# Kernel optimization log

Measured on AMD Instinct MI355X. Metric: run time of the kernel, lower is better.

The kernel has to match this reference:

```python
import jax, jax.numpy as jnp
import numpy as np

HIDDEN = 768
NUM_HEADS = 12
HEAD_DIM = HIDDEN // NUM_HEADS
B, S = 4, 2048


def setup_inputs() -> dict:
    key = jax.random.key(0)
    ks = jax.random.split(key, 10)
    scale = 1.0 / np.sqrt(HIDDEN)
    return {
        "hidden_states": jax.random.normal(ks[0], (B, S, HIDDEN), dtype=jnp.float32),
        "attention_mask": jnp.ones((B, S), dtype=jnp.float32),
        "Wq": jax.random.normal(ks[1], (HIDDEN, HIDDEN), dtype=jnp.float32) * scale,
        "bq": jnp.zeros((HIDDEN,), dtype=jnp.float32),
        "Wk": jax.random.normal(ks[2], (HIDDEN, HIDDEN), dtype=jnp.float32) * scale,
        "bk": jnp.zeros((HIDDEN,), dtype=jnp.float32),
        "Wv": jax.random.normal(ks[3], (HIDDEN, HIDDEN), dtype=jnp.float32) * scale,
        "bv": jnp.zeros((HIDDEN,), dtype=jnp.float32),
        "Wo": jax.random.normal(ks[4], (HIDDEN, HIDDEN), dtype=jnp.float32) * scale,
        "bo": jnp.zeros((HIDDEN,), dtype=jnp.float32),
    }


def reference(hidden_states, attention_mask, Wq, bq, Wk, bk, Wv, bv, Wo, bo):
    b, s, _ = hidden_states.shape
    # nn.Linear: x @ W.T + b  (W is [out, in])
    Q = hidden_states @ Wq.T + bq
    K = hidden_states @ Wk.T + bk
    V = hidden_states @ Wv.T + bv
    # [b, s, h*d] -> [b, h, s, d]
    Q = Q.reshape(b, s, NUM_HEADS, HEAD_DIM).transpose(0, 2, 1, 3)
    K = K.reshape(b, s, NUM_HEADS, HEAD_DIM).transpose(0, 2, 1, 3)
    V = V.reshape(b, s, NUM_HEADS, HEAD_DIM).transpose(0, 2, 1, 3)
    # scores: [b, h, s, s]
    scores = jnp.einsum("bhqd,bhkd->bhqk", Q, K) / jnp.sqrt(
        jnp.asarray(HEAD_DIM, dtype=Q.dtype))
    # mask: [b, s] -> additive bias broadcast over heads and query dim
    bias = (1.0 - attention_mask)[:, None, None, :] * -10000.0
    scores = scores + bias
    probs = jax.nn.softmax(scores, axis=-1)  # dropout p=0.0 -> identity
    context = jnp.einsum("bhqk,bhkd->bhqd", probs, V)
    context = context.transpose(0, 2, 1, 3).reshape(b, s, HIDDEN)
    return context @ Wo.T + bo
```

## Files before the change

kernel.cpp:

```cpp
#include <hip/hip_runtime.h>
#include <hip/hip_bf16.h>

#define SEQ   2048
#define NH    12
#define MTOK  8192

typedef __attribute__((ext_vector_type(8))) short short8;
typedef __attribute__((ext_vector_type(4))) short short4v;
typedef __attribute__((ext_vector_type(4))) float f32x4;

__device__ inline short f2bf(float x) {
  __hip_bfloat16 h = __float2bfloat16(x);
  return *(short*)&h;
}

#define GLL(gp, lp) __builtin_amdgcn_global_load_lds( \
    (const __attribute__((address_space(1))) void*)(gp), \
    (__attribute__((address_space(3))) void*)(lp), 16, 0, 0)

#define MFMA(a, b, c) __builtin_amdgcn_mfma_f32_16x16x32_bf16(a, b, c, 0, 0, 0)

#if !defined(__HIP_DEVICE_COMPILE__)
#define MFMA16(a, b, c) (c)
#elif __has_builtin(__builtin_amdgcn_mfma_f32_16x16x16bf16_1k)
#define MFMA16(a, b, c) __builtin_amdgcn_mfma_f32_16x16x16bf16_1k(a, b, c, 0, 0, 0)
#elif __has_builtin(__builtin_amdgcn_mfma_f32_16x16x16_bf16)
#define MFMA16(a, b, c) __builtin_amdgcn_mfma_f32_16x16x16_bf16(a, b, c, 0, 0, 0)
#else
#error "no 16x16x16 bf16 mfma builtin on device"
#endif

#if !defined(__HIP_DEVICE_COMPILE__)
#define EXP2(x) (x)
#elif __has_builtin(__builtin_amdgcn_exp2f)
#define EXP2(x) __builtin_amdgcn_exp2f(x)
#else
#define EXP2(x) __expf((x) * 0.6931471805599453f)
#endif

__device__ inline unsigned pack2bf(float a, float b) {
  unsigned ua = __float_as_uint(a) + 0x8000u;
  unsigned ub = __float_as_uint(b) + 0x8000u;
#if defined(__HIP_DEVICE_COMPILE__) && __has_builtin(__builtin_amdgcn_perm)
  return __builtin_amdgcn_perm(ub, ua, 0x07060302u);
#else
  return (ub & 0xFFFF0000u) | (ua >> 16);
#endif
}

union PackFrag {
  unsigned u[2];
  short4v s;
};

#define QSCALE 0.18033688011112042f
#define MBSCALE -14426.950408889634f

__global__ __launch_bounds__(256) void prep(
    const float* __restrict__ hs, const float* __restrict__ Wq,
    const float* __restrict__ Wk, const float* __restrict__ Wv,
    const float* __restrict__ Wo, const float* __restrict__ mask,
    short* __restrict__ Xb, short* __restrict__ Wqkvb,
    short* __restrict__ Wob, float* __restrict__ mbias) {
  int bid = blockIdx.x;
  if (bid < 6144) {
    int i = bid * 256 + threadIdx.x;
    float4 v = ((const float4*)hs)[i];
    short4v o;
    o[0] = f2bf(v.x); o[1] = f2bf(v.y); o[2] = f2bf(v.z); o[3] = f2bf(v.w);
    ((short4v*)Xb)[i] = o;
  } else if (bid < 6144 + 2304) {
    int idx = (bid - 6144) * 256 + threadIdx.x;
    int r = idx / 192, c = (idx - r * 192) * 4;
    const float* src;
    short* dst;
    int rr;
    if (r < 768)       { src = Wq; rr = r;        dst = Wqkvb; }
    else if (r < 1536) { src = Wk; rr = r - 768;  dst = Wqkvb; }
    else if (r < 2304) { src = Wv; rr = r - 1536; dst = Wqkvb; }
    else               { src = Wo; rr = r - 2304; dst = Wob; r = rr; }
    float4 v = *(const float4*)&src[(size_t)rr * 768 + c];
    short4v o;
    o[0] = f2bf(v.x); o[1] = f2bf(v.y); o[2] = f2bf(v.z); o[3] = f2bf(v.w);
    *(short4v*)&dst[(size_t)r * 768 + c] = o;
  } else {
    int i = (bid - 6144 - 2304) * 256 + threadIdx.x;
    if (i < MTOK) mbias[i] = (1.f - mask[i]) * MBSCALE;
  }
}

#define GEMM_BK64_LOOP(Aptr, Bptr)                                            \
  __shared__ __align__(16) short As[128 * 64];                                \
  __shared__ __align__(16) short Bs[128 * 64];                                \
  const int t = threadIdx.x;                                                  \
  const int wid = t >> 6, lane = t & 63, l15 = lane & 15, quad = lane >> 4;   \
  const int bm = blockIdx.x * 128, bn = blockIdx.y * 128;                     \
  const int mq = (wid & 1) * 64, nq = (wid >> 1) * 64;                        \
  const int srow8 = lane >> 3;                                                \
  const int schunk = lane & 7;                                                \
  const int scol = (schunk ^ srow8) * 8;                                      \
  f32x4 acc[4][4] = {};                                                       \
  const short *gA[4], *gB[4];                                                 \
  _Pragma("unroll") for (int g = 0; g < 4; ++g) {                             \
    int row = wid * 32 + g * 8 + srow8;                                       \
    gA[g] = (Aptr) + (size_t)(bm + row) * 768 + scol;                         \
    gB[g] = (Bptr) + (size_t)(bn + row) * 768 + scol;                         \
  }                                                                           \
  for (int k0 = 0; k0 < 768; k0 += 64) {                                      \
    _Pragma("unroll") for (int g = 0; g < 4; ++g)                             \
      GLL(gA[g] + k0, &As[(wid * 32 + g * 8) * 64]);                          \
    _Pragma("unroll") for (int g = 0; g < 4; ++g)                             \
      GLL(gB[g] + k0, &Bs[(wid * 32 + g * 8) * 64]);                          \
    __syncthreads();                                                          \
    _Pragma("unroll") for (int ks = 0; ks < 2; ++ks) {                        \
      short8 a[4], b[4];                                                      \
      _Pragma("unroll") for (int mt = 0; mt < 4; ++mt)                        \
        a[mt] = *(const short8*)&As[(mq + mt * 16 + l15) * 64 +               \
                                    (((ks * 4 + quad) ^ (l15 & 7)) * 8)];     \
      _Pragma("unroll") for (int nt = 0; nt < 4; ++nt)                        \
        b[nt] = *(const short8*)&Bs[(nq + nt * 16 + l15) * 64 +               \
                                    (((ks * 4 + quad) ^ (l15 & 7)) * 8)];     \
      _Pragma("unroll") for (int mt = 0; mt < 4; ++mt)                        \
        _Pragma("unroll") for (int nt = 0; nt < 4; ++nt)                      \
          acc[mt][nt] = MFMA(a[mt], b[nt], acc[mt][nt]);                      \
    }                                                                         \
    __syncthreads();                                                          \
  }

__global__ __launch_bounds__(256) void gemm_qkv(
    const short* __restrict__ A, const short* __restrict__ B,
    const float* __restrict__ bq, const float* __restrict__ bk,
    const float* __restrict__ bv, short* __restrict__ Qb,
    short* __restrict__ Kb, short* __restrict__ Vt) {
  GEMM_BK64_LOOP(A, B)

  const int seg = bn >= 1536 ? 2 : (bn >= 768 ? 1 : 0);
  const float* bias = seg == 0 ? bq : (seg == 1 ? bk : bv);
  const int colbase = bn - seg * 768;

  if (seg < 2) {
    short* dst = seg == 0 ? Qb : Kb;
    const float sc = seg == 0 ? QSCALE : 1.f;
#pragma unroll
    for (int mt = 0; mt < 4; ++mt)
#pragma unroll
      for (int nt = 0; nt < 4; ++nt) {
        int col = colbase + nq + nt * 16 + l15;
        float bias_v = bias[col];
#pragma unroll
        for (int i = 0; i < 4; ++i) {
          int row = bm + mq + mt * 16 + quad * 4 + i;
          dst[(size_t)row * 768 + col] = f2bf((acc[mt][nt][i] + bias_v) * sc);
        }
      }
  } else {
#pragma unroll
    for (int mt = 0; mt < 4; ++mt) {
      int row0 = bm + mq + mt * 16 + quad * 4;
      int b_ = row0 >> 11, s = row0 & 2047;
#pragma unroll
      for (int nt = 0; nt < 4; ++nt) {
        int col = colbase + nq + nt * 16 + l15;
        float bias_v = bias[col];
        int h = col >> 6, d = col & 63;
        short4v pv;
#pragma unroll
        for (int i = 0; i < 4; ++i) pv[i] = f2bf(acc[mt][nt][i] + bias_v);
        *(short4v*)&Vt[(((size_t)b_ * NH + h) * 64 + d) * 2048 + s] = pv;
      }
    }
  }
}

__global__ __launch_bounds__(256) void gemm_out(
    const short* __restrict__ A, const short* __restrict__ B,
    const float* __restrict__ bias, float* __restrict__ C) {
  GEMM_BK64_LOOP(A, B)

#pragma unroll
  for (int mt = 0; mt < 4; ++mt)
#pragma unroll
    for (int nt = 0; nt < 4; ++nt) {
      int col = bn + nq + nt * 16 + l15;
      float bias_v = bias[col];
#pragma unroll
      for (int i = 0; i < 4; ++i) {
        int row = bm + mq + mt * 16 + quad * 4 + i;
        C[(size_t)row * 768 + col] = acc[mt][nt][i] + bias_v;
      }
    }
}

__global__ __launch_bounds__(256, 3) void attn_v8(
    const short* __restrict__ Qb, const short* __restrict__ Kb,
    const short* __restrict__ Vt, const float* __restrict__ maskb,
    short* __restrict__ Ctx) {
  __shared__ __align__(16) short Ks[2][64 * 64];
  __shared__ __align__(16) short Vs[2][64 * 64];
  const int t = threadIdx.x;
  const int w = t >> 6, lane = t & 63, l15 = lane & 15, quad = lane >> 4;
  const int bh = blockIdx.x, b = bh / NH, h = bh % NH;
  const int q0 = blockIdx.y * 128;

  short8 qa[2][2];
#pragma unroll
  for (int qt = 0; qt < 2; ++qt)
#pragma unroll
    for (int ks = 0; ks < 2; ++ks) {
      int row = b * 2048 + q0 + w * 32 + qt * 16 + l15;
      qa[qt][ks] = *(const short8*)&Qb[(size_t)row * 768 + h * 64 + ks * 32 + quad * 8];
    }

  f32x4 O[2][4] = {};
  f32x4 lacc[2] = {};
  short4v ones4;
#pragma unroll
  for (int j = 0; j < 4; ++j) ones4[j] = (short)0x3F80;

  const int r0 = w * 16 + (lane >> 3);
  const int pc = lane & 7;
  const int swz0 = (pc ^ (r0 & 7)) * 8;
  const int swz1 = (pc ^ ((r0 + 8) & 7)) * 8;
  const short* gK0 = Kb + (size_t)(b * 2048 + r0) * 768 + h * 64 + swz0;
  const short* gK1 = Kb + (size_t)(b * 2048 + r0 + 8) * 768 + h * 64 + swz1;
  const short* gV0 = Vt + ((size_t)bh * 64 + r0) * 2048 + swz0;
  const short* gV1 = Vt + ((size_t)bh * 64 + r0 + 8) * 2048 + swz1;
  const float* mb = maskb + b * 2048;
  const int rs = l15 & 7;

  GLL(gK0, &Ks[0][(w * 16) * 64]);
  GLL(gK1, &Ks[0][(w * 16 + 8) * 64]);
  GLL(gV0, &Vs[0][(w * 16) * 64]);
  GLL(gV1, &Vs[0][(w * 16 + 8) * 64]);

  for (int ti = 0; ti < 32; ++ti) {
    const int cur = ti & 1;
    const int k0 = ti * 64;
    __syncthreads();

    {
      const size_t kn = (size_t)(((ti + 1) & 31) * 64);
      GLL(gK0 + kn * 768, &Ks[1 - cur][(w * 16) * 64]);
      GLL(gK1 + kn * 768, &Ks[1 - cur][(w * 16 + 8) * 64]);
      GLL(gV0 + kn, &Vs[1 - cur][(w * 16) * 64]);
      GLL(gV1 + kn, &Vs[1 - cur][(w * 16 + 8) * 64]);
    }

    f32x4 S[4][2] = {};
#pragma unroll
    for (int ks = 0; ks < 2; ++ks) {
      short8 kb[4];
#pragma unroll
      for (int kt = 0; kt < 4; ++kt)
        kb[kt] = *(const short8*)&Ks[cur][(kt * 16 + l15) * 64 +
                                         (((ks * 4 + quad) ^ rs) * 8)];
#pragma unroll
      for (int kt = 0; kt < 4; ++kt) {
        S[kt][0] = MFMA(kb[kt], qa[0][ks], S[kt][0]);
        S[kt][1] = MFMA(kb[kt], qa[1][ks], S[kt][1]);
      }
    }

    short4v pb[4][2];
#pragma unroll
    for (int kt = 0; kt < 4; ++kt) {
      float4 mb4 = *(const float4*)&mb[k0 + kt * 16 + quad * 4];
#pragma unroll
      for (int qt = 0; qt < 2; ++qt) {
        float p0 = EXP2(S[kt][qt][0] + mb4.x);
        float p1 = EXP2(S[kt][qt][1] + mb4.y);
        float p2 = EXP2(S[kt][qt][2] + mb4.z);
        float p3 = EXP2(S[kt][qt][3] + mb4.w);
        PackFrag pf;
        pf.u[0] = pack2bf(p0, p1);
        pf.u[1] = pack2bf(p2, p3);
        pb[kt][qt] = pf.s;
      }
    }

#pragma unroll
    for (int kt = 0; kt < 4; ++kt) {
      lacc[0] = MFMA16(ones4, pb[kt][0], lacc[0]);
      lacc[1] = MFMA16(ones4, pb[kt][1], lacc[1]);
    }

#pragma unroll
    for (int kt = 0; kt < 4; ++kt) {
#pragma unroll
      for (int dt = 0; dt < 4; ++dt) {
        short4v av = *(const short4v*)&Vs[cur][(dt * 16 + l15) * 64 +
            (((kt * 2 + (quad >> 1)) ^ rs) * 8) + (quad & 1) * 4];
        O[0][dt] = MFMA16(av, pb[kt][0], O[0][dt]);
        O[1][dt] = MFMA16(av, pb[kt][1], O[1][dt]);
      }
    }
  }

#pragma unroll
  for (int qt = 0; qt < 2; ++qt) {
    float inv = 1.f / lacc[qt][0];
    int row = b * 2048 + q0 + w * 32 + qt * 16 + l15;
#pragma unroll
    for (int dt = 0; dt < 4; ++dt) {
      PackFrag pf;
      pf.u[0] = pack2bf(O[qt][dt][0] * inv, O[qt][dt][1] * inv);
      pf.u[1] = pack2bf(O[qt][dt][2] * inv, O[qt][dt][3] * inv);
      *(short4v*)&Ctx[(size_t)row * 768 + h * 64 + dt * 16 + quad * 4] = pf.s;
    }
  }
}

extern "C" void kernel_launch(void* const* d_in, const int* in_sizes, int n_in,
                              void* d_out, int out_size, void* d_ws,
                              size_t ws_size, hipStream_t stream) {
  const float* hs   = (const float*)d_in[0];
  const float* mask = (const float*)d_in[1];
  const float* Wq   = (const float*)d_in[2];
  const float* bq   = (const float*)d_in[3];
  const float* Wk   = (const float*)d_in[4];
  const float* bk   = (const float*)d_in[5];
  const float* Wv   = (const float*)d_in[6];
  const float* bv   = (const float*)d_in[7];
  const float* Wo   = (const float*)d_in[8];
  const float* bo   = (const float*)d_in[9];

  char* ws = (char*)d_ws;
  short* Xb    = (short*)(ws);
  short* Wqkvb = (short*)(ws + 12582912);
  short* Wob   = (short*)(ws + 16121856);
  short* Qb    = (short*)(ws + 17301504);
  short* Kb    = (short*)(ws + 29884416);
  short* Vtg   = (short*)(ws + 42467328);
  short* Ctxb  = (short*)(ws + 55050240);
  float* mbias = (float*)(ws + 67633152);

  prep<<<8480, 256, 0, stream>>>(hs, Wq, Wk, Wv, Wo, mask,
                                 Xb, Wqkvb, Wob, mbias);
  gemm_qkv<<<dim3(64, 18), 256, 0, stream>>>(Xb, Wqkvb, bq, bk, bv,
                                             Qb, Kb, Vtg);
  attn_v8<<<dim3(48, 16), 256, 0, stream>>>(Qb, Kb, Vtg, mbias, Ctxb);
  gemm_out<<<dim3(64, 6), 256, 0, stream>>>(Ctxb, Wob, bo, (float*)d_out);
}
```

Measured before the change: 229.1 us.

## Halve attention query tile and drop K/V double buffering for higher occupancy

Each attention block now handles 64 query rows instead of 128 (one 16-row tile per wave), and the grid doubles to compensate. The K/V shared-memory tiles become single-buffered, so each iteration loads and then waits, with a second barrier before the next overwrite. Launch bounds rise to 6 blocks per CU. The aim is more resident waves to hide latency, at the cost of losing the prefetch overlap and doubling total K/V tile reads from global memory.

Measured after the change: 243.9 us. 1.06x slower.

```diff
diff --git a/kernel.cpp b/kernel.cpp
--- a/kernel.cpp
+++ b/kernel.cpp
@@ -191,28 +191,26 @@
     }
 }
 
-__global__ __launch_bounds__(256, 3) void attn_v8(
+__global__ __launch_bounds__(256, 6) void attn_v9(
     const short* __restrict__ Qb, const short* __restrict__ Kb,
     const short* __restrict__ Vt, const float* __restrict__ maskb,
     short* __restrict__ Ctx) {
-  __shared__ __align__(16) short Ks[2][64 * 64];
-  __shared__ __align__(16) short Vs[2][64 * 64];
+  __shared__ __align__(16) short Ks[64 * 64];
+  __shared__ __align__(16) short Vs[64 * 64];
   const int t = threadIdx.x;
   const int w = t >> 6, lane = t & 63, l15 = lane & 15, quad = lane >> 4;
   const int bh = blockIdx.x, b = bh / NH, h = bh % NH;
-  const int q0 = blockIdx.y * 128;
-
-  short8 qa[2][2];
-#pragma unroll
-  for (int qt = 0; qt < 2; ++qt)
-#pragma unroll
-    for (int ks = 0; ks < 2; ++ks) {
-      int row = b * 2048 + q0 + w * 32 + qt * 16 + l15;
-      qa[qt][ks] = *(const short8*)&Qb[(size_t)row * 768 + h * 64 + ks * 32 + quad * 8];
-    }
-
-  f32x4 O[2][4] = {};
-  f32x4 lacc[2] = {};
+  const int q0 = blockIdx.y * 64;
+
+  short8 qa[2];
+#pragma unroll
+  for (int ks = 0; ks < 2; ++ks) {
+    int row = b * 2048 + q0 + w * 16 + l15;
+    qa[ks] = *(const short8*)&Qb[(size_t)row * 768 + h * 64 + ks * 32 + quad * 8];
+  }
+
+  f32x4 O[4] = {};
+  f32x4 lacc = {};
   short4v ones4;
 #pragma unroll
   for (int j = 0; j < 4; ++j) ones4[j] = (short)0x3F80;
@@ -228,83 +226,64 @@
   const float* mb = maskb + b * 2048;
   const int rs = l15 & 7;
 
-  GLL(gK0, &Ks[0][(w * 16) * 64]);
-  GLL(gK1, &Ks[0][(w * 16 + 8) * 64]);
-  GLL(gV0, &Vs[0][(w * 16) * 64]);
-  GLL(gV1, &Vs[0][(w * 16 + 8) * 64]);
-
-  for (int ti = 0; ti < 32; ++ti) {
-    const int cur = ti & 1;
-    const int k0 = ti * 64;
+  for (int k0 = 0; k0 < SEQ; k0 += 64) {
+    GLL(gK0 + (size_t)k0 * 768, &Ks[(w * 16) * 64]);
+    GLL(gK1 + (size_t)k0 * 768, &Ks[(w * 16 + 8) * 64]);
+    GLL(gV0 + k0, &Vs[(w * 16) * 64]);
+    GLL(gV1 + k0, &Vs[(w * 16 + 8) * 64]);
     __syncthreads();
 
-    {
-      const size_t kn = (size_t)(((ti + 1) & 31) * 64);
-      GLL(gK0 + kn * 768, &Ks[1 - cur][(w * 16) * 64]);
-      GLL(gK1 + kn * 768, &Ks[1 - cur][(w * 16 + 8) * 64]);
-      GLL(gV0 + kn, &Vs[1 - cur][(w * 16) * 64]);
-      GLL(gV1 + kn, &Vs[1 - cur][(w * 16 + 8) * 64]);
-    }
-
-    f32x4 S[4][2] = {};
+    f32x4 S[4] = {};
 #pragma unroll
     for (int ks = 0; ks < 2; ++ks) {
       short8 kb[4];
 #pragma unroll
       for (int kt = 0; kt < 4; ++kt)
-        kb[kt] = *(const short8*)&Ks[cur][(kt * 16 + l15) * 64 +
-                                         (((ks * 4 + quad) ^ rs) * 8)];
-#pragma unroll
-      for (int kt = 0; kt < 4; ++kt) {
-        S[kt][0] = MFMA(kb[kt], qa[0][ks], S[kt][0]);
-        S[kt][1] = MFMA(kb[kt], qa[1][ks], S[kt][1]);
-      }
-    }
-
-    short4v pb[4][2];
+        kb[kt] = *(const short8*)&Ks[(kt * 16 + l15) * 64 +
+                                     (((ks * 4 + quad) ^ rs) * 8)];
+#pragma unroll
+      for (int kt = 0; kt < 4; ++kt)
+        S[kt] = MFMA(kb[kt], qa[ks], S[kt]);
+    }
+
+    short4v pb[4];
 #pragma unroll
     for (int kt = 0; kt < 4; ++kt) {
       float4 mb4 = *(const float4*)&mb[k0 + kt * 16 + quad * 4];
-#pragma unroll
-      for (int qt = 0; qt < 2; ++qt) {
-        float p0 = EXP2(S[kt][qt][0] + mb4.x);
-        float p1 = EXP2(S[kt][qt][1] + mb4.y);
-        float p2 = EXP2(S[kt][qt][2] + mb4.z);
-        float p3 = EXP2(S[kt][qt][3] + mb4.w);
-        PackFrag pf;
-        pf.u[0] = pack2bf(p0, p1);
-        pf.u[1] = pack2bf(p2, p3);
-        pb[kt][qt] = pf.s;
+      float p0 = EXP2(S[kt][0] + mb4.x);
+      float p1 = EXP2(S[kt][1] + mb4.y);
+      float p2 = EXP2(S[kt][2] + mb4.z);
+      float p3 = EXP2(S[kt][3] + mb4.w);
+      PackFrag pf;
+      pf.u[0] = pack2bf(p0, p1);
+      pf.u[1] = pack2bf(p2, p3);
+      pb[kt] = pf.s;
+    }
+
+#pragma unroll
+    for (int kt = 0; kt < 4; ++kt)
+      lacc = MFMA16(ones4, pb[kt], lacc);
+
+#pragma unroll
+    for (int kt = 0; kt < 4; ++kt) {
+#pragma unroll
+      for (int dt = 0; dt < 4; ++dt) {
+        short4v av = *(const short4v*)&Vs[(dt * 16 + l15) * 64 +
+            (((kt * 2 + (quad >> 1)) ^ rs) * 8) + (quad & 1) * 4];
+        O[dt] = MFMA16(av, pb[kt], O[dt]);
       }
     }
-
-#pragma unroll
-    for (int kt = 0; kt < 4; ++kt) {
-      lacc[0] = MFMA16(ones4, pb[kt][0], lacc[0]);
-      lacc[1] = MFMA16(ones4, pb[kt][1], lacc[1]);
-    }
-
-#pragma unroll
-    for (int kt = 0; kt < 4; ++kt) {
-#pragma unroll
-      for (int dt = 0; dt < 4; ++dt) {
-        short4v av = *(const short4v*)&Vs[cur][(dt * 16 + l15) * 64 +
-            (((kt * 2 + (quad >> 1)) ^ rs) * 8) + (quad & 1) * 4];
-        O[0][dt] = MFMA16(av, pb[kt][0], O[0][dt]);
-        O[1][dt] = MFMA16(av, pb[kt][1], O[1][dt]);
-      }
-    }
-  }
-
-#pragma unroll
-  for (int qt = 0; qt < 2; ++qt) {
-    float inv = 1.f / lacc[qt][0];
-    int row = b * 2048 + q0 + w * 32 + qt * 16 + l15;
+    __syncthreads();
+  }
+
+  {
+    float inv = 1.f / lacc[0];
+    int row = b * 2048 + q0 + w * 16 + l15;
 #pragma unroll
     for (int dt = 0; dt < 4; ++dt) {
       PackFrag pf;
-      pf.u[0] = pack2bf(O[qt][dt][0] * inv, O[qt][dt][1] * inv);
-      pf.u[1] = pack2bf(O[qt][dt][2] * inv, O[qt][dt][3] * inv);
+      pf.u[0] = pack2bf(O[dt][0] * inv, O[dt][1] * inv);
+      pf.u[1] = pack2bf(O[dt][2] * inv, O[dt][3] * inv);
       *(short4v*)&Ctx[(size_t)row * 768 + h * 64 + dt * 16 + quad * 4] = pf.s;
     }
   }
@@ -338,6 +317,6 @@
                                  Xb, Wqkvb, Wob, mbias);
   gemm_qkv<<<dim3(64, 18), 256, 0, stream>>>(Xb, Wqkvb, bq, bk, bv,
                                              Qb, Kb, Vtg);
-  attn_v8<<<dim3(48, 16), 256, 0, stream>>>(Qb, Kb, Vtg, mbias, Ctxb);
+  attn_v9<<<dim3(48, 32), 256, 0, stream>>>(Qb, Kb, Vtg, mbias, Ctxb);
   gemm_out<<<dim3(64, 6), 256, 0, stream>>>(Ctxb, Wob, bo, (float*)d_out);
 }
```
